# Performance work log

Hardware: AMD Instinct MI355X
Metric: run time of the kernel (lower is better)

Reference implementation:

```python
import jax, jax.numpy as jnp
import numpy as np

N_LAYERS = 2
D_MODEL = 1024
EXPAND = 2
D_INNER = EXPAND * D_MODEL   # 2048
D_STATE = 16
D_CONV = 4
DT_RANK = (D_MODEL + 15) // 16  # 64
BATCH = 2
SEQ = 1024


def setup_inputs() -> dict:
    key = jax.random.key(0)
    ks = jax.random.split(key, 8)
    x = jax.random.normal(ks[0], (BATCH, SEQ, D_MODEL), jnp.float32)
    in_proj_w = jax.random.normal(ks[1], (N_LAYERS, 2 * D_INNER, D_MODEL), jnp.float32) * 0.02
    conv_w = jax.random.normal(ks[2], (N_LAYERS, D_INNER, 1, D_CONV), jnp.float32) * 0.2
    conv_b = jnp.zeros((N_LAYERS, D_INNER), jnp.float32)
    x_proj_w = jax.random.normal(ks[3], (N_LAYERS, DT_RANK + 2 * D_STATE, D_INNER), jnp.float32) * 0.02
    dt_proj_w = jax.random.normal(ks[4], (N_LAYERS, D_INNER, DT_RANK), jnp.float32) * 0.1
    # softplus(b) ~ 0.01 -> realistic small dt init
    dt_proj_b = jnp.full((N_LAYERS, D_INNER), float(np.log(np.expm1(0.01))), jnp.float32)
    A_log = jnp.tile(jnp.log(jnp.arange(1, D_STATE + 1, dtype=jnp.float32))[None, None, :], (N_LAYERS, D_INNER, 1))
    D = jnp.ones((N_LAYERS, D_INNER), jnp.float32)
    out_proj_w = jax.random.normal(ks[5], (N_LAYERS, D_MODEL, D_INNER), jnp.float32) * 0.02
    return {
        'x': x, 'in_proj_w': in_proj_w, 'conv_w': conv_w, 'conv_b': conv_b,
        'x_proj_w': x_proj_w, 'dt_proj_w': dt_proj_w, 'dt_proj_b': dt_proj_b,
        'A_log': A_log, 'D': D, 'out_proj_w': out_proj_w,
    }


def _mamba_block(x, W_in, w_c, b_c, W_x, W_dt, b_dt, A_log, Dp, W_out):
    # x: (B, L, d_model)
    xz = jnp.einsum('bld,ed->ble', x, W_in)           # (B, L, 2*d_inner)
    xc, z = jnp.split(xz, 2, axis=-1)
    # causal depthwise conv1d over time
    xc = xc.transpose(0, 2, 1)                         # (B, d_inner, L)
    xc = jax.lax.conv_general_dilated(
        xc, w_c, window_strides=(1,), padding=[(D_CONV - 1, 0)],
        dimension_numbers=('NCH', 'OIH', 'NCH'), feature_group_count=D_INNER,
    ) + b_c[None, :, None]
    u = jax.nn.silu(xc).transpose(0, 2, 1)             # (B, L, d_inner)
    # input-dependent dt, B, C
    x_dbl = jnp.einsum('bld,ed->ble', u, W_x)          # (B, L, dt_rank+2N)
    dt, Bm, Cm = jnp.split(x_dbl, [DT_RANK, DT_RANK + D_STATE], axis=-1)
    delta = jax.nn.softplus(jnp.einsum('blr,dr->bld', dt, W_dt) + b_dt)  # (B, L, d_inner)
    A = -jnp.exp(A_log)                                 # (d_inner, N)
    dA = jnp.exp(jnp.einsum('bld,dn->bldn', delta, A))  # (B, L, d_inner, N)
    dBu = jnp.einsum('bld,bln,bld->bldn', delta, Bm, u) # (B, L, d_inner, N)

    def step(h, inp):
        dA_t, dBu_t, C_t = inp                          # (B,d,N), (B,d,N), (B,N)
        h = dA_t * h + dBu_t
        return h, jnp.einsum('bdn,bn->bd', h, C_t)

    h0 = jnp.zeros((x.shape[0], D_INNER, D_STATE), x.dtype)
    _, ys = jax.lax.scan(step, h0, (dA.transpose(1, 0, 2, 3), dBu.transpose(1, 0, 2, 3), Cm.transpose(1, 0, 2)))
    y = ys.transpose(1, 0, 2) + u * Dp                  # (B, L, d_inner)
    y = y * jax.nn.silu(z)
    return jnp.einsum('bld,od->blo', y, W_out)          # (B, L, d_model)


def _forward(x, in_proj_w, conv_w, conv_b, x_proj_w, dt_proj_w, dt_proj_b, A_log, D, out_proj_w):
    residual = x
    for i in range(N_LAYERS):
        x = _mamba_block(x, in_proj_w[i], conv_w[i], conv_b[i], x_proj_w[i],
                         dt_proj_w[i], dt_proj_b[i], A_log[i], D[i], out_proj_w[i])
    return x + residual


def reference(x, in_proj_w, conv_w, conv_b, x_proj_w, dt_proj_w, dt_proj_b, A_log, D, out_proj_w):
    return _forward(x, in_proj_w, conv_w, conv_b, x_proj_w, dt_proj_w, dt_proj_b, A_log, D, out_proj_w)
```

## Files before the change

kernel.cpp:

```cpp
#include <hip/hip_runtime.h>
#include <hip/hip_bf16.h>

#define NLAYERS 2
#define DMODEL 1024
#define DINNER 2048
#define DSTATE 16
#define DCONV 4
#define DTRANK 64
#define BATCH 2
#define SEQ 1024
#define TOK (BATCH * SEQ)

#define NCHUNK 32
#define CLEN (SEQ / NCHUNK)
#define KSX 16
#define KSO 4

typedef short bf16x8 __attribute__((ext_vector_type(8)));
typedef float f32x4 __attribute__((ext_vector_type(4)));
typedef unsigned short ushort8 __attribute__((ext_vector_type(8)));

__device__ __forceinline__ float softplusf(float x) {
    return (x > 20.f) ? x : log1pf(__expf(x));
}
__device__ __forceinline__ float siluf(float x) {
    return x / (1.f + __expf(-x));
}
__device__ __forceinline__ unsigned short f2bf(float f) {
    union { float f; unsigned int u; } v; v.f = f;
    const unsigned int r = (v.u + 0x7FFFu + ((v.u >> 16) & 1u)) >> 16;
    return (unsigned short)r;
}
__device__ __forceinline__ float bf2f(unsigned short s) {
    union { unsigned int u; float f; } v; v.u = ((unsigned int)s) << 16;
    return v.f;
}

__device__ __forceinline__ void cvt8(const float* __restrict__ in,
                                     unsigned short* __restrict__ out, int i) {
    const float4 a = reinterpret_cast<const float4*>(in)[i * 2 + 0];
    const float4 b = reinterpret_cast<const float4*>(in)[i * 2 + 1];
    ushort4 o0, o1;
    o0.x = f2bf(a.x); o0.y = f2bf(a.y); o0.z = f2bf(a.z); o0.w = f2bf(a.w);
    o1.x = f2bf(b.x); o1.y = f2bf(b.y); o1.z = f2bf(b.z); o1.w = f2bf(b.w);
    reinterpret_cast<ushort4*>(out)[i * 2 + 0] = o0;
    reinterpret_cast<ushort4*>(out)[i * 2 + 1] = o1;
}

#define WI8 1048576
#define WO8 524288
#define WX8 49152
#define WD8 32768
#define AC8 262144
__global__ __launch_bounds__(256)
void cvt_all(const float* __restrict__ wi, const float* __restrict__ wo,
             const float* __restrict__ wx, const float* __restrict__ wd,
             const float* __restrict__ xin,
             unsigned short* __restrict__ wi_bf, unsigned short* __restrict__ wo_bf,
             unsigned short* __restrict__ wx_bf, unsigned short* __restrict__ wd_bf,
             unsigned short* __restrict__ act_bf) {
    int i = blockIdx.x * 256 + threadIdx.x;
    if (i < WI8) { cvt8(wi, wi_bf, i); return; }
    i -= WI8;
    if (i < WO8) { cvt8(wo, wo_bf, i); return; }
    i -= WO8;
    if (i < WX8) { cvt8(wx, wx_bf, i); return; }
    i -= WX8;
    if (i < WD8) { cvt8(wd, wd_bf, i); return; }
    i -= WD8;
    if (i < AC8) { cvt8(xin, act_bf, i); return; }
}

template <int EPI>
__global__ __launch_bounds__(256)
void gemm_bf16(const unsigned short* __restrict__ Ab, int lda,
               const unsigned short* __restrict__ Wb, int ldw,
               void* __restrict__ Cptr, int ldc, int kLen, int Nw,
               size_t cSlice, const float* __restrict__ bias) {
    __shared__ unsigned short As[2][128 * 32];
    __shared__ unsigned short Bs[2][128 * 32];
    const int tid = threadIdx.x;
    const int wave = tid >> 6, lane = tid & 63;
    const int wr = wave >> 1, wc = wave & 1;
    const int m0 = blockIdx.y * 128, n0 = blockIdx.x * 128;
    const int kbeg = blockIdx.z * kLen;
    const int r = lane & 15, kq = lane >> 4;
    const int nt = kLen >> 5;

    const int ch0 = tid, ch1 = 256 + tid;
    const int sm0 = ch0 >> 2, sk0 = (ch0 & 3) * 8;
    const int sm1 = ch1 >> 2, sk1 = (ch1 & 3) * 8;
    const int wrow0 = min(n0 + sm0, Nw - 1);
    const int wrow1 = min(n0 + sm1, Nw - 1);

    auto stage = [&](int buf, int kt) {
        __builtin_amdgcn_global_load_lds(
            (const __attribute__((address_space(1))) void*)
                &Ab[(size_t)(m0 + sm0) * lda + kt + sk0],
            (__attribute__((address_space(3))) void*)&As[buf][ch0 * 8], 16, 0, 0);
        __builtin_amdgcn_global_load_lds(
            (const __attribute__((address_space(1))) void*)
                &Wb[(size_t)wrow0 * ldw + kt + sk0],
            (__attribute__((address_space(3))) void*)&Bs[buf][ch0 * 8], 16, 0, 0);
        __builtin_amdgcn_global_load_lds(
            (const __attribute__((address_space(1))) void*)
                &Ab[(size_t)(m0 + sm1) * lda + kt + sk1],
            (__attribute__((address_space(3))) void*)&As[buf][ch1 * 8], 16, 0, 0);
        __builtin_amdgcn_global_load_lds(
            (const __attribute__((address_space(1))) void*)
                &Wb[(size_t)wrow1 * ldw + kt + sk1],
            (__attribute__((address_space(3))) void*)&Bs[buf][ch1 * 8], 16, 0, 0);
    };

    f32x4 acc[4][4] = {};
    stage(0, kbeg);
    for (int t = 0; t < nt; ++t) {
        const int cur = t & 1;
        if (t + 1 < nt) {
            stage(cur ^ 1, kbeg + (t + 1) * 32);
            asm volatile("s_waitcnt vmcnt(4)" ::: "memory");
        } else {
            asm volatile("s_waitcnt vmcnt(0)" ::: "memory");
        }
        __builtin_amdgcn_s_barrier();
        __builtin_amdgcn_sched_barrier(0);
        bf16x8 a[4], b[4];
#pragma unroll
        for (int f = 0; f < 4; ++f) {
            a[f] = *reinterpret_cast<const bf16x8*>(
                &As[cur][(wr * 64 + f * 16 + r) * 32 + kq * 8]);
            b[f] = *reinterpret_cast<const bf16x8*>(
                &Bs[cur][(wc * 64 + f * 16 + r) * 32 + kq * 8]);
        }
#pragma unroll
        for (int fi = 0; fi < 4; ++fi)
#pragma unroll
            for (int fj = 0; fj < 4; ++fj)
                acc[fi][fj] = __builtin_amdgcn_mfma_f32_16x16x32_bf16(
                    a[fi], b[fj], acc[fi][fj], 0, 0, 0);
        __builtin_amdgcn_sched_barrier(0);
        asm volatile("s_waitcnt lgkmcnt(0)" ::: "memory");
        __builtin_amdgcn_s_barrier();
    }

    const int cr = lane >> 4, cc = lane & 15;
#pragma unroll
    for (int fi = 0; fi < 4; ++fi)
#pragma unroll
        for (int fj = 0; fj < 4; ++fj)
#pragma unroll
            for (int p = 0; p < 4; ++p) {
                const int m = m0 + wr * 64 + fi * 16 + cr * 4 + p;
                const int n = n0 + wc * 64 + fj * 16 + cc;
                const float v = acc[fi][fj][p];
                if (EPI == 0) {
                    if (n < Nw)
                        ((float*)Cptr)[(size_t)blockIdx.z * cSlice +
                                       (size_t)m * ldc + n] = v;
                } else if (EPI == 3) {
                    ((unsigned short*)Cptr)[(size_t)blockIdx.z * cSlice +
                                            (size_t)m * ldc + n] = f2bf(v);
                } else {
                    ((unsigned short*)Cptr)[(size_t)m * ldc + n] =
                        f2bf(softplusf(v + bias[n]));
                }
            }
}

__global__ __launch_bounds__(256)
void conv_silu8(const unsigned short* __restrict__ xz_bf,
                const float* __restrict__ cw,
                const float* __restrict__ cb,
                unsigned short* __restrict__ u_bf) {
    const int gid = blockIdx.x * 256 + threadIdx.x;
    const int d8 = gid & 255;
    const int t = gid >> 8;
    const int l = t & (SEQ - 1);
    const int d0 = d8 * 8;

    float cwv[8][4];
#pragma unroll
    for (int j = 0; j < 8; ++j) {
        const float4 c = *reinterpret_cast<const float4*>(&cw[(d0 + j) * DCONV]);
        cwv[j][0] = c.x; cwv[j][1] = c.y; cwv[j][2] = c.z; cwv[j][3] = c.w;
    }
    float acc[8];
    {
        const float4 b0 = *reinterpret_cast<const float4*>(&cb[d0]);
        const float4 b1 = *reinterpret_cast<const float4*>(&cb[d0 + 4]);
        acc[0] = b0.x; acc[1] = b0.y; acc[2] = b0.z; acc[3] = b0.w;
        acc[4] = b1.x; acc[5] = b1.y; acc[6] = b1.z; acc[7] = b1.w;
    }
#pragma unroll
    for (int k = 0; k < DCONV; ++k) {
        const int li = l - (DCONV - 1) + k;
        if (li >= 0) {
            const ushort8 v = *reinterpret_cast<const ushort8*>(
                &xz_bf[(size_t)(t - (DCONV - 1) + k) * 4096 + d0]);
#pragma unroll
            for (int j = 0; j < 8; ++j)
                acc[j] = fmaf(cwv[j][k], bf2f(v[j]), acc[j]);
        }
    }
    ushort8 o;
#pragma unroll
    for (int j = 0; j < 8; ++j) o[j] = f2bf(siluf(acc[j]));
    *reinterpret_cast<ushort8*>(&u_bf[(size_t)t * DINNER + d0]) = o;
}

__global__ __launch_bounds__(256)
void reduce_x(const float* __restrict__ part, float* __restrict__ xdbl,
              unsigned short* __restrict__ dt_bf) {
    const int i = blockIdx.x * 256 + threadIdx.x;
    if (i >= TOK * 96) return;
    float s = 0.f;
#pragma unroll
    for (int k = 0; k < KSX; ++k) s += part[(size_t)k * (TOK * 96) + i];
    xdbl[i] = s;
    const int t = i / 96, c = i - t * 96;
    if (c < DTRANK) dt_bf[t * DTRANK + c] = f2bf(s);
}

template <int MODE>
__global__ __launch_bounds__(256)
void reduce_out(const unsigned short* __restrict__ part,
                const float* __restrict__ resid, void* __restrict__ outp) {
    const int i = blockIdx.x * 256 + threadIdx.x;
    if (i >= TOK * DMODEL / 4) return;
    float s[4] = {0.f, 0.f, 0.f, 0.f};
#pragma unroll
    for (int k = 0; k < KSO; ++k) {
        const ushort4 p = reinterpret_cast<const ushort4*>(
            &part[(size_t)k * (TOK * DMODEL)])[i];
        s[0] += bf2f(p.x); s[1] += bf2f(p.y); s[2] += bf2f(p.z); s[3] += bf2f(p.w);
    }
    if (MODE == 0) {
        ushort4 o;
        o.x = f2bf(s[0]); o.y = f2bf(s[1]); o.z = f2bf(s[2]); o.w = f2bf(s[3]);
        reinterpret_cast<ushort4*>(outp)[i] = o;
    } else {
        const float4 rr = reinterpret_cast<const float4*>(resid)[i];
        float4 o;
        o.x = s[0] + rr.x; o.y = s[1] + rr.y; o.z = s[2] + rr.z; o.w = s[3] + rr.w;
        reinterpret_cast<float4*>(outp)[i] = o;
    }
}

__device__ __forceinline__ void load_b16(const float* __restrict__ p, float* B) {
    const float4* bp = reinterpret_cast<const float4*>(p);
    const float4 b0 = bp[0], b1 = bp[1], b2 = bp[2], b3 = bp[3];
    B[0] = b0.x; B[1] = b0.y; B[2] = b0.z; B[3] = b0.w;
    B[4] = b1.x; B[5] = b1.y; B[6] = b1.z; B[7] = b1.w;
    B[8] = b2.x; B[9] = b2.y; B[10] = b2.z; B[11] = b2.w;
    B[12] = b3.x; B[13] = b3.y; B[14] = b3.z; B[15] = b3.w;
}
__device__ __forceinline__ void load_bf16x16(const unsigned short* __restrict__ p,
                                             float* B) {
    const ushort8 v0 = *reinterpret_cast<const ushort8*>(p);
    const ushort8 v1 = *reinterpret_cast<const ushort8*>(p + 8);
#pragma unroll
    for (int j = 0; j < 8; ++j) { B[j] = bf2f(v0[j]); B[8 + j] = bf2f(v1[j]); }
}
__device__ __forceinline__ void store_bf16x16(unsigned short* __restrict__ p,
                                              const float* B) {
    ushort8 v0, v1;
#pragma unroll
    for (int j = 0; j < 8; ++j) { v0[j] = f2bf(B[j]); v1[j] = f2bf(B[8 + j]); }
    *reinterpret_cast<ushort8*>(p) = v0;
    *reinterpret_cast<ushort8*>(p + 8) = v1;
}

__global__ __launch_bounds__(256)
void scan_partial(const unsigned short* __restrict__ delta_bf,
                  const unsigned short* __restrict__ u_bf,
                  const float* __restrict__ xdbl,
                  const float* __restrict__ A_log,
                  unsigned short* __restrict__ hbuf,
                  unsigned short* __restrict__ Pbuf) {
    const int b = blockIdx.y / NCHUNK;
    const int c = blockIdx.y % NCHUNK;
    const int d = blockIdx.x * 256 + threadIdx.x;
    const int t0 = b * SEQ + c * CLEN;

    float A_dn[16];
    load_b16(&A_log[d * DSTATE], A_dn);
#pragma unroll
    for (int n = 0; n < 16; ++n) A_dn[n] = -__expf(A_dn[n]);

    float h[16], P[16];
#pragma unroll
    for (int n = 0; n < 16; ++n) { h[n] = 0.f; P[n] = 1.f; }

    float dltA, uvA, BA[16];
    float dltB, uvB, BB[16];
    dltA = bf2f(delta_bf[(size_t)t0 * DINNER + d]);
    uvA = bf2f(u_bf[(size_t)t0 * DINNER + d]);
    load_b16(&xdbl[(size_t)t0 * 96 + DTRANK], BA);

#define PSTEP(dlt_, uv_, Bc_)                              \
    {                                                      \
        const float du = (dlt_) * (uv_);                   \
        _Pragma("unroll")                                  \
        for (int n = 0; n < 16; ++n) {                     \
            const float dA = __expf((dlt_) * A_dn[n]);     \
            h[n] = fmaf(dA, h[n], du * Bc_[n]);            \
            P[n] *= dA;                                    \
        }                                                  \
    }

    for (int l = 0; l < CLEN; l += 2) {
        const int t = t0 + l;
        dltB = bf2f(delta_bf[(size_t)(t + 1) * DINNER + d]);
        uvB = bf2f(u_bf[(size_t)(t + 1) * DINNER + d]);
        load_b16(&xdbl[(size_t)(t + 1) * 96 + DTRANK], BB);
        PSTEP(dltA, uvA, BA);
        if (l + 2 < CLEN) {
            dltA = bf2f(delta_bf[(size_t)(t + 2) * DINNER + d]);
            uvA = bf2f(u_bf[(size_t)(t + 2) * DINNER + d]);
            load_b16(&xdbl[(size_t)(t + 2) * 96 + DTRANK], BA);
        }
        PSTEP(dltB, uvB, BB);
    }
#undef PSTEP

    const size_t base = ((size_t)(b * NCHUNK + c) * DINNER + d) * DSTATE;
    store_bf16x16(&hbuf[base], h);
    store_bf16x16(&Pbuf[base], P);
}

__global__ __launch_bounds__(256)
void scan_combine(unsigned short* __restrict__ hbuf,
                  const unsigned short* __restrict__ Pbuf) {
    const int gid = blockIdx.x * 256 + threadIdx.x;
    const int b = gid / (DINNER * DSTATE);
    const int dn = gid - b * (DINNER * DSTATE);
    const size_t base = (size_t)b * NCHUNK * DINNER * DSTATE + dn;
    float hi = 0.f;
#pragma unroll
    for (int c = 0; c < NCHUNK; ++c) {
        const size_t idx = base + (size_t)c * (DINNER * DSTATE);
        const float hl = bf2f(hbuf[idx]);
        const float Pc = bf2f(Pbuf[idx]);
        hbuf[idx] = f2bf(hi);
        hi = fmaf(Pc, hi, hl);
    }
}

__global__ __launch_bounds__(256)
void scan_final(const unsigned short* __restrict__ delta_bf,
                const unsigned short* __restrict__ u_bf,
                const float* __restrict__ xdbl,
                const unsigned short* __restrict__ xz_bf,
                const float* __restrict__ A_log,
                const float* __restrict__ Dp,
                const unsigned short* __restrict__ hbuf,
                unsigned short* __restrict__ yout) {
    const int b = blockIdx.y / NCHUNK;
    const int c = blockIdx.y % NCHUNK;
    const int d = blockIdx.x * 256 + threadIdx.x;
    const int t0 = b * SEQ + c * CLEN;

    float A_dn[16];
    load_b16(&A_log[d * DSTATE], A_dn);
#pragma unroll
    for (int n = 0; n < 16; ++n) A_dn[n] = -__expf(A_dn[n]);
    const float Dd = Dp[d];

    float h[16];
    load_bf16x16(&hbuf[((size_t)(b * NCHUNK + c) * DINNER + d) * DSTATE], h);

    float dltA, uvA, BA[16], CA[16];
    float dltB, uvB, BB[16], CB[16];
    dltA = bf2f(delta_bf[(size_t)t0 * DINNER + d]);
    uvA = bf2f(u_bf[(size_t)t0 * DINNER + d]);
    load_b16(&xdbl[(size_t)t0 * 96 + DTRANK], BA);
    load_b16(&xdbl[(size_t)t0 * 96 + DTRANK + DSTATE], CA);

#define FSTEP(t_, dlt_, uv_, Bc_, Cc_)                          \
    {                                                           \
        const float du = (dlt_) * (uv_);                        \
        _Pragma("unroll")                                       \
        for (int n = 0; n < 16; ++n) {                          \
            const float dA = __expf((dlt_) * A_dn[n]);          \
            h[n] = fmaf(dA, h[n], du * Bc_[n]);                 \
        }                                                       \
        float s0 = 0.f, s1 = 0.f, s2 = 0.f, s3 = 0.f;           \
        _Pragma("unroll")                                       \
        for (int q = 0; q < 4; ++q) {                           \
            s0 = fmaf(h[q*4+0], Cc_[q*4+0], s0);                \
            s1 = fmaf(h[q*4+1], Cc_[q*4+1], s1);                \
            s2 = fmaf(h[q*4+2], Cc_[q*4+2], s2);                \
            s3 = fmaf(h[q*4+3], Cc_[q*4+3], s3);                \
        }                                                       \
        const float zv = bf2f(xz_bf[(size_t)(t_) * 4096 + 2048 + d]); \
        const float y = (s0 + s1) + (s2 + s3) + (uv_) * Dd;     \
        yout[(size_t)(t_) * DINNER + d] = f2bf(y * siluf(zv));  \
    }

    for (int l = 0; l < CLEN; l += 2) {
        const int t = t0 + l;
        dltB = bf2f(delta_bf[(size_t)(t + 1) * DINNER + d]);
        uvB = bf2f(u_bf[(size_t)(t + 1) * DINNER + d]);
        load_b16(&xdbl[(size_t)(t + 1) * 96 + DTRANK], BB);
        load_b16(&xdbl[(size_t)(t + 1) * 96 + DTRANK + DSTATE], CB);
        FSTEP(t, dltA, uvA, BA, CA);
        if (l + 2 < CLEN) {
            dltA = bf2f(delta_bf[(size_t)(t + 2) * DINNER + d]);
            uvA = bf2f(u_bf[(size_t)(t + 2) * DINNER + d]);
            load_b16(&xdbl[(size_t)(t + 2) * 96 + DTRANK], BA);
            load_b16(&xdbl[(size_t)(t + 2) * 96 + DTRANK + DSTATE], CA);
        }
        FSTEP(t + 1, dltB, uvB, BB, CB);
    }
#undef FSTEP
}

extern "C" void kernel_launch(void* const* d_in, const int* in_sizes, int n_in,
                              void* d_out, int out_size, void* d_ws, size_t ws_size,
                              hipStream_t stream) {
    const float* x          = (const float*)d_in[0];
    const float* in_proj_w  = (const float*)d_in[1];
    const float* conv_w     = (const float*)d_in[2];
    const float* conv_b     = (const float*)d_in[3];
    const float* x_proj_w   = (const float*)d_in[4];
    const float* dt_proj_w  = (const float*)d_in[5];
    const float* dt_proj_b  = (const float*)d_in[6];
    const float* A_log      = (const float*)d_in[7];
    const float* Dp         = (const float*)d_in[8];
    const float* out_proj_w = (const float*)d_in[9];
    float* out = (float*)d_out;

    float* ws = (float*)d_ws;
    float* xpart = ws;
    float* xdbl  = xpart + 3145728;
    unsigned short* us = (unsigned short*)(xdbl + 196608);
    unsigned short* hbuf   = us;
    unsigned short* Pbuf   = hbuf + 2097152;
    unsigned short* opart  = Pbuf + 2097152;
    unsigned short* wi_bf  = opart + 8388608;
    unsigned short* wo_bf  = wi_bf + 8388608;
    unsigned short* wx_bf  = wo_bf + 4194304;
    unsigned short* wd_bf  = wx_bf + 393216;
    unsigned short* xz_bf  = wd_bf + 262144;
    unsigned short* u_bf   = xz_bf + 8388608;
    unsigned short* dlt_bf = u_bf  + 4194304;
    unsigned short* act_bf = dlt_bf + 4194304;
    unsigned short* y_bf   = act_bf + 2097152;
    unsigned short* dt_bf  = y_bf  + 4194304;

    cvt_all<<<(WI8 + WO8 + WX8 + WD8 + AC8 + 255) / 256, 256, 0, stream>>>(
        in_proj_w, out_proj_w, x_proj_w, dt_proj_w, x,
        wi_bf, wo_bf, wx_bf, wd_bf, act_bf);

    for (int layer = 0; layer < NLAYERS; ++layer) {
        const unsigned short* Wi = wi_bf + (size_t)layer * (2 * DINNER) * DMODEL;
        const unsigned short* Wo = wo_bf + (size_t)layer * DMODEL * DINNER;
        const unsigned short* Wx = wx_bf + (size_t)layer * 96 * DINNER;
        const unsigned short* Wd = wd_bf + (size_t)layer * DINNER * DTRANK;
        const float* cw = conv_w    + (size_t)layer * DINNER * DCONV;
        const float* cb = conv_b    + (size_t)layer * DINNER;
        const float* bd = dt_proj_b + (size_t)layer * DINNER;
        const float* Al = A_log     + (size_t)layer * DINNER * DSTATE;
        const float* Dl = Dp        + (size_t)layer * DINNER;

        {
            dim3 grid(4096 / 128, TOK / 128, 1);
            gemm_bf16<3><<<grid, 256, 0, stream>>>(act_bf, DMODEL, Wi, DMODEL,
                                                   xz_bf, 2 * DINNER, DMODEL,
                                                   2 * DINNER, 0, nullptr);
        }
        conv_silu8<<<(TOK * 256) / 256, 256, 0, stream>>>(xz_bf, cw, cb, u_bf);
        {
            dim3 grid(1, TOK / 128, KSX);
            gemm_bf16<0><<<grid, 256, 0, stream>>>(u_bf, DINNER, Wx, DINNER,
                                                   xpart, 96, DINNER / KSX, 96,
                                                   (size_t)TOK * 96, nullptr);
            reduce_x<<<(TOK * 96 + 255) / 256, 256, 0, stream>>>(xpart, xdbl, dt_bf);
        }
        {
            dim3 grid(DINNER / 128, TOK / 128, 1);
            gemm_bf16<4><<<grid, 256, 0, stream>>>(dt_bf, DTRANK, Wd, DTRANK,
                                                   dlt_bf, DINNER, DTRANK, DINNER,
                                                   0, bd);
        }
        {
            dim3 gridA(DINNER / 256, BATCH * NCHUNK);
            scan_partial<<<gridA, 256, 0, stream>>>(dlt_bf, u_bf, xdbl, Al,
                                                    hbuf, Pbuf);
            scan_combine<<<(BATCH * DINNER * DSTATE) / 256, 256, 0, stream>>>(hbuf, Pbuf);
            scan_final<<<gridA, 256, 0, stream>>>(dlt_bf, u_bf, xdbl, xz_bf,
                                                  Al, Dl, hbuf, y_bf);
        }
        {
            dim3 grid(DMODEL / 128, TOK / 128, KSO);
            gemm_bf16<3><<<grid, 256, 0, stream>>>(y_bf, DINNER, Wo, DINNER,
                                                   opart, DMODEL, DINNER / KSO,
                                                   DMODEL, (size_t)TOK * DMODEL,
                                                   nullptr);
            const int nred = TOK * DMODEL / 4;
            if (layer == NLAYERS - 1) {
                reduce_out<1><<<(nred + 255) / 256, 256, 0, stream>>>(opart, x, out);
            } else {
                reduce_out<0><<<(nred + 255) / 256, 256, 0, stream>>>(opart, nullptr,
                                                                      act_bf);
            }
        }
    }
}
```

Measured before the change: 325.0 us.

## Triple-buffer GEMM loads, bf16 split-K partials, cheaper scan chunk decay

Result: no change. 324.4 us (-0.2%).

```diff
diff --git a/kernel.cpp b/kernel.cpp
--- a/kernel.cpp
+++ b/kernel.cpp
@@ -77,8 +77,8 @@
                const unsigned short* __restrict__ Wb, int ldw,
                void* __restrict__ Cptr, int ldc, int kLen, int Nw,
                size_t cSlice, const float* __restrict__ bias) {
-    __shared__ unsigned short As[2][128 * 32];
-    __shared__ unsigned short Bs[2][128 * 32];
+    __shared__ unsigned short As[3][128 * 32];
+    __shared__ unsigned short Bs[3][128 * 32];
     const int tid = threadIdx.x;
     const int wave = tid >> 6, lane = tid & 63;
     const int wr = wave >> 1, wc = wave & 1;
@@ -114,10 +114,13 @@
 
     f32x4 acc[4][4] = {};
     stage(0, kbeg);
+    if (nt > 1) stage(1, kbeg + 32);
     for (int t = 0; t < nt; ++t) {
-        const int cur = t & 1;
-        if (t + 1 < nt) {
-            stage(cur ^ 1, kbeg + (t + 1) * 32);
+        const int cur = t % 3;
+        if (t + 2 < nt) {
+            stage((t + 2) % 3, kbeg + (t + 2) * 32);
+            asm volatile("s_waitcnt vmcnt(8)" ::: "memory");
+        } else if (t + 1 < nt) {
             asm volatile("s_waitcnt vmcnt(4)" ::: "memory");
         } else {
             asm volatile("s_waitcnt vmcnt(0)" ::: "memory");
@@ -160,9 +163,13 @@
                 } else if (EPI == 3) {
                     ((unsigned short*)Cptr)[(size_t)blockIdx.z * cSlice +
                                             (size_t)m * ldc + n] = f2bf(v);
-                } else {
+                } else if (EPI == 4) {
                     ((unsigned short*)Cptr)[(size_t)m * ldc + n] =
                         f2bf(softplusf(v + bias[n]));
+                } else {
+                    if (n < Nw)
+                        ((unsigned short*)Cptr)[(size_t)blockIdx.z * cSlice +
+                                                (size_t)m * ldc + n] = f2bf(v);
                 }
             }
 }
@@ -209,13 +216,13 @@
 }
 
 __global__ __launch_bounds__(256)
-void reduce_x(const float* __restrict__ part, float* __restrict__ xdbl,
+void reduce_x(const unsigned short* __restrict__ part, float* __restrict__ xdbl,
               unsigned short* __restrict__ dt_bf) {
     const int i = blockIdx.x * 256 + threadIdx.x;
     if (i >= TOK * 96) return;
     float s = 0.f;
 #pragma unroll
-    for (int k = 0; k < KSX; ++k) s += part[(size_t)k * (TOK * 96) + i];
+    for (int k = 0; k < KSX; ++k) s += bf2f(part[(size_t)k * (TOK * 96) + i]);
     xdbl[i] = s;
     const int t = i / 96, c = i - t * 96;
     if (c < DTRANK) dt_bf[t * DTRANK + c] = f2bf(s);
@@ -287,9 +294,10 @@
 #pragma unroll
     for (int n = 0; n < 16; ++n) A_dn[n] = -__expf(A_dn[n]);
 
-    float h[16], P[16];
-#pragma unroll
-    for (int n = 0; n < 16; ++n) { h[n] = 0.f; P[n] = 1.f; }
+    float h[16];
+#pragma unroll
+    for (int n = 0; n < 16; ++n) h[n] = 0.f;
+    float sdlt = 0.f;
 
     float dltA, uvA, BA[16];
     float dltB, uvB, BB[16];
@@ -300,11 +308,11 @@
 #define PSTEP(dlt_, uv_, Bc_)                              \
     {                                                      \
         const float du = (dlt_) * (uv_);                   \
+        sdlt += (dlt_);                                    \
         _Pragma("unroll")                                  \
         for (int n = 0; n < 16; ++n) {                     \
             const float dA = __expf((dlt_) * A_dn[n]);     \
             h[n] = fmaf(dA, h[n], du * Bc_[n]);            \
-            P[n] *= dA;                                    \
         }                                                  \
     }
 
@@ -323,6 +331,10 @@
     }
 #undef PSTEP
 
+    float P[16];
+#pragma unroll
+    for (int n = 0; n < 16; ++n) P[n] = __expf(sdlt * A_dn[n]);
+
     const size_t base = ((size_t)(b * NCHUNK + c) * DINNER + d) * DSTATE;
     store_bf16x16(&hbuf[base], h);
     store_bf16x16(&Pbuf[base], P);
@@ -335,14 +347,19 @@
     const int b = gid / (DINNER * DSTATE);
     const int dn = gid - b * (DINNER * DSTATE);
     const size_t base = (size_t)b * NCHUNK * DINNER * DSTATE + dn;
-    float hi = 0.f;
+    float hv[NCHUNK], Pv[NCHUNK];
 #pragma unroll
     for (int c = 0; c < NCHUNK; ++c) {
         const size_t idx = base + (size_t)c * (DINNER * DSTATE);
-        const float hl = bf2f(hbuf[idx]);
-        const float Pc = bf2f(Pbuf[idx]);
+        hv[c] = bf2f(hbuf[idx]);
+        Pv[c] = bf2f(Pbuf[idx]);
+    }
+    float hi = 0.f;
+#pragma unroll
+    for (int c = 0; c < NCHUNK; ++c) {
+        const size_t idx = base + (size_t)c * (DINNER * DSTATE);
         hbuf[idx] = f2bf(hi);
-        hi = fmaf(Pc, hi, hl);
+        hi = fmaf(Pv[c], hi, hv[c]);
     }
 }
 
@@ -431,10 +448,10 @@
     float* out = (float*)d_out;
 
     float* ws = (float*)d_ws;
-    float* xpart = ws;
-    float* xdbl  = xpart + 3145728;
+    float* xdbl  = ws;
     unsigned short* us = (unsigned short*)(xdbl + 196608);
-    unsigned short* hbuf   = us;
+    unsigned short* xpart  = us;
+    unsigned short* hbuf   = xpart + 3145728;
     unsigned short* Pbuf   = hbuf + 2097152;
     unsigned short* opart  = Pbuf + 2097152;
     unsigned short* wi_bf  = opart + 8388608;
@@ -472,7 +489,7 @@
         conv_silu8<<<(TOK * 256) / 256, 256, 0, stream>>>(xz_bf, cw, cb, u_bf);
         {
             dim3 grid(1, TOK / 128, KSX);
-            gemm_bf16<0><<<grid, 256, 0, stream>>>(u_bf, DINNER, Wx, DINNER,
+            gemm_bf16<5><<<grid, 256, 0, stream>>>(u_bf, DINNER, Wx, DINNER,
                                                    xpart, 96, DINNER / KSX, 96,
                                                    (size_t)TOK * 96, nullptr);
             reduce_x<<<(TOK * 96 + 255) / 256, 256, 0, stream>>>(xpart, xdbl, dt_bf);
```
